# Optimization experiments

Hardware: AMD Instinct MI355X
Metric: run time of the kernel (lower is better)

## Reference

```python
import jax, jax.numpy as jnp
import numpy as np
import math

D_MODEL = 1024
N_HEADS = 16
D_FF = 4096
B, S = 4, 2048
EPS = 1e-5


def _layernorm(x, g, b):
    mu = jnp.mean(x, axis=-1, keepdims=True)
    var = jnp.mean(jnp.square(x - mu), axis=-1, keepdims=True)
    return (x - mu) * jax.lax.rsqrt(var + EPS) * g + b


def setup_inputs() -> dict:
    key = jax.random.key(0)
    ks = jax.random.split(key, 16)
    D, F = D_MODEL, D_FF
    s = 1.0 / math.sqrt(D)
    sf = 1.0 / math.sqrt(F)
    return {
        "x": jax.random.normal(ks[0], (B, S, D), jnp.float32),
        "mask": jnp.ones((B, 1, 1, S), jnp.int32),
        "Wq": jax.random.uniform(ks[1], (D, D), jnp.float32, -s, s),
        "bq": jnp.zeros((D,), jnp.float32),
        "Wk": jax.random.uniform(ks[2], (D, D), jnp.float32, -s, s),
        "bk": jnp.zeros((D,), jnp.float32),
        "Wv": jax.random.uniform(ks[3], (D, D), jnp.float32, -s, s),
        "bv": jnp.zeros((D,), jnp.float32),
        "Wo": jax.random.uniform(ks[4], (D, D), jnp.float32, -s, s),
        "bo": jnp.zeros((D,), jnp.float32),
        "W1": jax.random.uniform(ks[5], (D, F), jnp.float32, -s, s),
        "b1": jnp.zeros((F,), jnp.float32),
        "W2": jax.random.uniform(ks[6], (F, D), jnp.float32, -sf, sf),
        "b2": jnp.zeros((D,), jnp.float32),
        "g1": jnp.ones((D,), jnp.float32),
        "be1": jnp.zeros((D,), jnp.float32),
        "g2": jnp.ones((D,), jnp.float32),
        "be2": jnp.zeros((D,), jnp.float32),
    }


def reference(x, mask, Wq, bq, Wk, bk, Wv, bv, Wo, bo, W1, b1, W2, b2, g1, be1, g2, be2):
    Bb, Ss, D = x.shape
    H = N_HEADS
    hd = D // H
    # QKV projections -> [B, H, S, hd]
    q = (x @ Wq + bq).reshape(Bb, Ss, H, hd).transpose(0, 2, 1, 3)
    k = (x @ Wk + bk).reshape(Bb, Ss, H, hd).transpose(0, 2, 1, 3)
    v = (x @ Wv + bv).reshape(Bb, Ss, H, hd).transpose(0, 2, 1, 3)
    # explicit O(S^2) attention, as in the source
    scores = jnp.einsum("bhqd,bhkd->bhqk", q, k) / math.sqrt(hd)
    scores = jnp.where(mask == 0, jnp.float32(-1e9), scores)
    attn = jax.nn.softmax(scores, axis=-1)
    o = jnp.einsum("bhqk,bhkd->bhqd", attn, v)
    o = o.transpose(0, 2, 1, 3).reshape(Bb, Ss, D)
    attn_out = o @ Wo + bo
    # residual + LN (dropout in eval mode = identity)
    h = _layernorm(x + attn_out, g1, be1)
    ff = jax.nn.relu(h @ W1 + b1) @ W2 + b2
    return _layernorm(h + ff, g2, be2)
```

## Files before the change

kernel.cpp:

```cpp
#include <hip/hip_runtime.h>
#include <hip/hip_bf16.h>
#include <stdint.h>

typedef __bf16 bf16;
typedef __bf16 bf16x8 __attribute__((ext_vector_type(8)));
typedef __bf16 bf16x4 __attribute__((ext_vector_type(4)));
typedef float f32x4 __attribute__((ext_vector_type(4)));
typedef unsigned short u16;

__device__ __forceinline__ float b2f(bf16 v) { return (float)v; }
__device__ __forceinline__ bf16 f2b(float f) { return (bf16)f; }

#define GLD16(gp, lp)                                              \
  __builtin_amdgcn_global_load_lds(                                \
      (const __attribute__((address_space(1))) void*)(gp),         \
      (__attribute__((address_space(3))) void*)(lp), 16, 0, 0)

__device__ __forceinline__ float ldval(const void* p, size_t i, int isf32) {
  return isf32 ? ((const float*)p)[i] : b2f(((const bf16*)p)[i]);
}

__global__ void sniff_kernel(const void* x, int* flag) {
  __shared__ int smax[256];
  int tid = threadIdx.x;
  const u16* p = (const u16*)x;
  int mx = 0;
  for (int i = tid; i < 8192; i += 256) {
    int e = (p[i] >> 7) & 0xFF;
    mx = mx > e ? mx : e;
  }
  smax[tid] = mx;
  __syncthreads();
  for (int s = 128; s > 0; s >>= 1) {
    if (tid < s) smax[tid] = smax[tid] > smax[tid + s] ? smax[tid] : smax[tid + s];
    __syncthreads();
  }
  if (tid == 0) *flag = (smax[0] >= 135) ? 1 : 0;
}

__global__ void cvt_kernel(const void* __restrict__ in, bf16* __restrict__ out,
                           int n, const int* __restrict__ flag) {
  int f = *flag;
  int i = blockIdx.x * 256 + threadIdx.x;
  if (i < n) out[i] = f2b(ldval(in, i, f));
}

__global__ void cvt_biases_kernel(const void* bq, const void* bk, const void* bv,
                                  const void* bo, const void* b1, const void* b2,
                                  const void* g1, const void* be1, const void* g2,
                                  const void* be2, bf16* __restrict__ sv,
                                  const int* __restrict__ flag) {
  int f = *flag;
  int i = blockIdx.x * 256 + threadIdx.x;
  if (i >= 13312) return;
  int seg = i >> 10;
  int off = i & 1023;
  const void* src;
  switch (seg) {
    case 0: src = bq; break;
    case 1: src = bk; break;
    case 2: src = bv; break;
    case 3: src = bo; break;
    case 4: case 5: case 6: case 7: src = b1; off = i - 4096; break;
    case 8: src = b2; break;
    case 9: src = g1; break;
    case 10: src = be1; break;
    case 11: src = g2; break;
    default: src = be2; break;
  }
  sv[i] = f2b(ldval(src, off, f));
}

__global__ void transpose_all(const void* Wq, const void* Wk, const void* Wv,
                              const void* Wo, const void* W1, const void* W2,
                              bf16* WqkvT, bf16* WoT, bf16* W1T, bf16* W2T,
                              const int* __restrict__ flag) {
  int f = *flag;
  __shared__ bf16 tile[32][33];
  int blk = blockIdx.x;
  const void* in; bf16* out; int K, N, bx, by;
  if (blk < 4096) {
    int w = blk >> 10, t = blk & 1023;
    bx = t & 31; by = t >> 5; K = 1024; N = 1024;
    if (w == 0)      { in = Wq; out = WqkvT; }
    else if (w == 1) { in = Wk; out = WqkvT + 1024 * 1024; }
    else if (w == 2) { in = Wv; out = WqkvT + 2048 * 1024; }
    else             { in = Wo; out = WoT; }
  } else if (blk < 8192) {
    int t = blk - 4096; bx = t & 127; by = t >> 7; K = 1024; N = 4096;
    in = W1; out = W1T;
  } else {
    int t = blk - 8192; bx = t & 31; by = t >> 5; K = 4096; N = 1024;
    in = W2; out = W2T;
  }
  int bn = bx * 32, bk = by * 32;
  int tx = threadIdx.x, ty = threadIdx.y;
#pragma unroll
  for (int i = 0; i < 32; i += 8)
    tile[ty + i][tx] = f2b(ldval(in, (size_t)(bk + ty + i) * N + bn + tx, f));
  __syncthreads();
#pragma unroll
  for (int i = 0; i < 32; i += 8)
    out[(size_t)(bn + ty + i) * K + bk + tx] = tile[tx][ty + i];
}

template <int ACT, int GROUP>
__global__ __launch_bounds__(256, 3)
void gemm_bt(const bf16* __restrict__ A, const bf16* __restrict__ Bt,
             const bf16* __restrict__ bias, bf16* __restrict__ C,
             int M, int N, int K) {
  __shared__ __attribute__((aligned(16))) bf16 As[128][64];
  __shared__ __attribute__((aligned(16))) bf16 Bs[128][64];
  __shared__ __attribute__((aligned(16))) bf16 Cs[32][136];
  const int tid = threadIdx.x;
  const int wave = tid >> 6;
  const int lane = tid & 63;

  const int grid_n = N >> 7;
  const int pid = blockIdx.x;
  const int xcd = pid & 7;
  const int j = pid >> 3;
  const int per = GROUP * grid_n;
  const int chunk = j / per;
  const int r0 = j - chunk * per;
  const int mb = xcd * 8 + chunk * GROUP + (r0 & (GROUP - 1));
  const int nb = r0 / GROUP;
  const int m0 = mb * 128;
  const int n0 = nb * 128;

  const int wr = (wave >> 1) * 64;
  const int wc = (wave & 1) * 64;
  const int row_q = lane & 15;
  const int quad = lane >> 4;

  const f32x4 fz = {0.f, 0.f, 0.f, 0.f};
  f32x4 acc[4][4];
#pragma unroll
  for (int i = 0; i < 4; i++)
#pragma unroll
    for (int jj = 0; jj < 4; jj++) acc[i][jj] = fz;

  int srow[4], sck[4];
#pragma unroll
  for (int i = 0; i < 4; i++) {
    int c = i * 256 + tid;
    srow[i] = c >> 3;
    sck[i] = (c & 7) * 8;
  }

  for (int k0 = 0; k0 < K; k0 += 64) {
    __syncthreads();
#pragma unroll
    for (int i = 0; i < 4; i++) {
      GLD16(A + (size_t)(m0 + srow[i]) * K + k0 + sck[i], &As[srow[i]][sck[i]]);
      GLD16(Bt + (size_t)(n0 + srow[i]) * K + k0 + sck[i], &Bs[srow[i]][sck[i]]);
    }
    __syncthreads();
#pragma unroll
    for (int ks = 0; ks < 2; ks++) {
      bf16x8 af[4], bfr[4];
      int cf = ks * 4 + quad;
#pragma unroll
      for (int mi = 0; mi < 4; mi++)
        af[mi] = *(const bf16x8*)&As[wr + mi * 16 + row_q][cf * 8];
#pragma unroll
      for (int ni = 0; ni < 4; ni++)
        bfr[ni] = *(const bf16x8*)&Bs[wc + ni * 16 + row_q][cf * 8];
#pragma unroll
      for (int mi = 0; mi < 4; mi++)
#pragma unroll
        for (int ni = 0; ni < 4; ni++)
          acc[mi][ni] = __builtin_amdgcn_mfma_f32_16x16x32_bf16(
              af[mi], bfr[ni], acc[mi][ni], 0, 0, 0);
    }
  }

#pragma unroll
  for (int p = 0; p < 4; p++) {
    __syncthreads();
    if ((wave >> 1) == (p >> 1)) {
#pragma unroll
      for (int ni = 0; ni < 4; ni++) {
        int col = wc + ni * 16 + row_q;
        float bval = b2f(bias[n0 + col]);
#pragma unroll
        for (int mi2 = 0; mi2 < 2; mi2++) {
          int mi = (p & 1) * 2 + mi2;
#pragma unroll
          for (int reg = 0; reg < 4; reg++) {
            int lr = mi2 * 16 + quad * 4 + reg;
            float v = acc[mi][ni][reg] + bval;
            if (ACT == 1) v = v > 0.f ? v : 0.f;
            Cs[lr][col] = f2b(v);
          }
        }
      }
    }
    __syncthreads();
#pragma unroll
    for (int i = 0; i < 2; i++) {
      int u = i * 256 + tid;
      int row = u >> 4;
      int cu = u & 15;
      uint4 v = *(const uint4*)&Cs[row][cu * 8];
      *(uint4*)&C[(size_t)(m0 + p * 32 + row) * N + n0 + cu * 8] = v;
    }
  }
}

template <int GROUP>
__global__ __launch_bounds__(256, 3)
void gemm_btv(const bf16* __restrict__ A, const bf16* __restrict__ Bt,
              const bf16* __restrict__ bias, bf16* __restrict__ Vg,
              int M, int N, int K) {
  __shared__ __attribute__((aligned(16))) bf16 As[128][64];
  __shared__ __attribute__((aligned(16))) bf16 Bs[128][64];
  __shared__ __attribute__((aligned(16))) bf16 Ct[32][136];
  const int tid = threadIdx.x;
  const int wave = tid >> 6;
  const int lane = tid & 63;

  const int grid_n = N >> 7;
  const int pid = blockIdx.x;
  const int xcd = pid & 7;
  const int j = pid >> 3;
  const int per = GROUP * grid_n;
  const int chunk = j / per;
  const int r0 = j - chunk * per;
  const int mb = xcd * 8 + chunk * GROUP + (r0 & (GROUP - 1));
  const int nb = r0 / GROUP;
  const int m0 = mb * 128;
  const int n0 = nb * 128;

  const int wr = (wave >> 1) * 64;
  const int wc = (wave & 1) * 64;
  const int row_q = lane & 15;
  const int quad = lane >> 4;

  const f32x4 fz = {0.f, 0.f, 0.f, 0.f};
  f32x4 acc[4][4];
#pragma unroll
  for (int i = 0; i < 4; i++)
#pragma unroll
    for (int jj = 0; jj < 4; jj++) acc[i][jj] = fz;

  int srow[4], sck[4];
#pragma unroll
  for (int i = 0; i < 4; i++) {
    int c = i * 256 + tid;
    srow[i] = c >> 3;
    sck[i] = (c & 7) * 8;
  }

  for (int k0 = 0; k0 < K; k0 += 64) {
    __syncthreads();
#pragma unroll
    for (int i = 0; i < 4; i++) {
      GLD16(A + (size_t)(m0 + srow[i]) * K + k0 + sck[i], &As[srow[i]][sck[i]]);
      GLD16(Bt + (size_t)(n0 + srow[i]) * K + k0 + sck[i], &Bs[srow[i]][sck[i]]);
    }
    __syncthreads();
#pragma unroll
    for (int ks = 0; ks < 2; ks++) {
      bf16x8 af[4], bfr[4];
      int cf = ks * 4 + quad;
#pragma unroll
      for (int mi = 0; mi < 4; mi++)
        af[mi] = *(const bf16x8*)&As[wr + mi * 16 + row_q][cf * 8];
#pragma unroll
      for (int ni = 0; ni < 4; ni++)
        bfr[ni] = *(const bf16x8*)&Bs[wc + ni * 16 + row_q][cf * 8];
#pragma unroll
      for (int mi = 0; mi < 4; mi++)
#pragma unroll
        for (int ni = 0; ni < 4; ni++)
          acc[mi][ni] = __builtin_amdgcn_mfma_f32_16x16x32_bf16(
              af[mi], bfr[ni], acc[mi][ni], 0, 0, 0);
    }
  }

  const int b = m0 >> 11;
  const int s0 = m0 & 2047;
#pragma unroll
  for (int p = 0; p < 4; p++) {
    __syncthreads();
    if ((wave & 1) == (p >> 1)) {
#pragma unroll
      for (int ni2 = 0; ni2 < 2; ni2++) {
        int ni = (p & 1) * 2 + ni2;
        int cl = ni2 * 16 + row_q;
        float bval = b2f(bias[n0 + p * 32 + cl]);
#pragma unroll
        for (int mi = 0; mi < 4; mi++)
#pragma unroll
          for (int reg = 0; reg < 4; reg++) {
            int row = wr + mi * 16 + quad * 4 + reg;
            Ct[cl][row] = f2b(acc[mi][ni][reg] + bval);
          }
      }
    }
    __syncthreads();
#pragma unroll
    for (int i = 0; i < 2; i++) {
      int u = i * 256 + tid;
      int cl = u >> 4;
      int rc = u & 15;
      uint4 v = *(const uint4*)&Ct[cl][rc * 8];
      *(uint4*)&Vg[(size_t)(b * 1024 + n0 + p * 32 + cl) * 2048 + s0 + rc * 8] = v;
    }
  }
}

#define BC 128
__global__ __launch_bounds__(256, 3)
void attn_kernel(const bf16* __restrict__ QKb, const bf16* __restrict__ Vg,
                 const int* __restrict__ mask, bf16* __restrict__ O) {
  __shared__ __attribute__((aligned(16))) bf16 Ks[BC][64];
  __shared__ __attribute__((aligned(16))) bf16 Vt[64][128];
  __shared__ __attribute__((aligned(16))) bf16 Ps[4][16][136];
  const int tid = threadIdx.x;
  const int wave = tid >> 6, lane = tid & 63;
  const int pid = blockIdx.x;
  const int xcd = pid & 7;
  const int jj = pid >> 3;
  const int bh = xcd * 8 + (jj >> 5);
  const int b = bh >> 4, h = bh & 15;
  const int q0 = (jj & 31) * 64;
  const int row_q = lane & 15, quad = lane >> 4;

  bf16x8 qf[2];
  {
    int qrow = q0 + wave * 16 + row_q;
    const bf16* qp = QKb + (size_t)(b * 2048 + qrow) * 2048 + h * 64 + quad * 8;
    qf[0] = *(const bf16x8*)qp;
    qf[1] = *(const bf16x8*)(qp + 32);
#pragma unroll
    for (int ks = 0; ks < 2; ks++)
#pragma unroll
      for (int e = 0; e < 8; e++) qf[ks][e] = f2b(b2f(qf[ks][e]) * 0.125f);
  }
  float m_i = -1e30f, l_i = 0.f;
  const f32x4 fz = {0.f, 0.f, 0.f, 0.f};
  f32x4 o_acc[4];
#pragma unroll
  for (int d = 0; d < 4; d++) o_acc[d] = fz;

  int ki[4], kdc[4], ksc[4], vd[4], vkc[4], vsc[4];
#pragma unroll
  for (int j = 0; j < 4; j++) {
    int c = j * 256 + tid;
    ki[j] = c >> 3;  kdc[j] = c & 7;   ksc[j] = (c & 7) ^ (ki[j] & 7);
    vd[j] = c >> 4;  vkc[j] = c & 15;  vsc[j] = (c & 15) ^ (vd[j] & 7);
  }
  const bf16* Kbase = QKb + (size_t)b * 2048 * 2048 + 1024 + h * 64;
  const bf16* Vbase = Vg + (size_t)(b * 1024 + h * 64) * 2048;
  const int* mrow = mask + b * 2048;
  const int swz = row_q & 7;

  for (int kb = 0; kb < 2048 / BC; kb++) {
    __syncthreads();
#pragma unroll
    for (int j = 0; j < 4; j++)
      GLD16(Kbase + (size_t)(kb * BC + ki[j]) * 2048 + ksc[j] * 8,
            &Ks[ki[j]][kdc[j] * 8]);
#pragma unroll
    for (int j = 0; j < 4; j++)
      GLD16(Vbase + (size_t)vd[j] * 2048 + kb * BC + vsc[j] * 8,
            &Vt[vd[j]][vkc[j] * 8]);
    __syncthreads();
    int2 mm = *(const int2*)&mrow[kb * BC + lane * 2];
    bool allok = (__ballot((mm.x != 0) & (mm.y != 0)) == ~0ull);

    f32x4 sacc[8];
#pragma unroll
    for (int nt = 0; nt < 8; nt++) sacc[nt] = fz;
#pragma unroll
    for (int ks = 0; ks < 2; ks++) {
      int kcf = ((ks * 4 + quad) ^ swz) * 8;
#pragma unroll
      for (int nt = 0; nt < 8; nt++) {
        bf16x8 kf = *(const bf16x8*)&Ks[nt * 16 + row_q][kcf];
        sacc[nt] = __builtin_amdgcn_mfma_f32_16x16x32_bf16(kf, qf[ks], sacc[nt], 0, 0, 0);
      }
    }
    if (!allok) {
#pragma unroll
      for (int nt = 0; nt < 8; nt++) {
        int4 m4 = *(const int4*)&mrow[kb * BC + nt * 16 + quad * 4];
#pragma unroll
        for (int r = 0; r < 4; r++)
          if (((const int*)&m4)[r] == 0) sacc[nt][r] = -1e9f;
      }
    }
    float mq[8];
#pragma unroll
    for (int nt = 0; nt < 8; nt++)
      mq[nt] = fmaxf(fmaxf(sacc[nt][0], sacc[nt][1]),
                     fmaxf(sacc[nt][2], sacc[nt][3]));
    float mx = fmaxf(fmaxf(fmaxf(mq[0], mq[1]), fmaxf(mq[2], mq[3])),
                     fmaxf(fmaxf(mq[4], mq[5]), fmaxf(mq[6], mq[7])));
    mx = fmaxf(mx, __shfl_xor(mx, 16));
    mx = fmaxf(mx, __shfl_xor(mx, 32));
    if (!__all(mx - m_i <= 5.0f)) {
      float mnew = fmaxf(m_i, mx);
      float alpha = __expf(m_i - mnew);
      m_i = mnew;
      l_i *= alpha;
      float al[4];
#pragma unroll
      for (int r = 0; r < 4; r++) al[r] = __shfl(alpha, quad * 4 + r);
#pragma unroll
      for (int d = 0; d < 4; d++)
#pragma unroll
        for (int r = 0; r < 4; r++) o_acc[d][r] *= al[r];
    }
    float rs = 0.f;
#pragma unroll
    for (int nt = 0; nt < 8; nt++) {
      float p0 = __expf(sacc[nt][0] - m_i);
      float p1 = __expf(sacc[nt][1] - m_i);
      float p2 = __expf(sacc[nt][2] - m_i);
      float p3 = __expf(sacc[nt][3] - m_i);
      rs += (p0 + p1) + (p2 + p3);
      bf16x4 pv = {f2b(p0), f2b(p1), f2b(p2), f2b(p3)};
      *(bf16x4*)&Ps[wave][row_q][nt * 16 + quad * 4] = pv;
    }
    rs += __shfl_xor(rs, 16);
    rs += __shfl_xor(rs, 32);
    l_i += rs;
#pragma unroll
    for (int kst = 0; kst < 4; kst++) {
      bf16x8 pf = *(const bf16x8*)&Ps[wave][row_q][kst * 32 + quad * 8];
      int vcf = ((kst * 4 + quad) ^ swz) * 8;
#pragma unroll
      for (int d = 0; d < 4; d++) {
        bf16x8 vf = *(const bf16x8*)&Vt[d * 16 + row_q][vcf];
        o_acc[d] = __builtin_amdgcn_mfma_f32_16x16x32_bf16(pf, vf, o_acc[d], 0, 0, 0);
      }
    }
  }
  float lv[4];
#pragma unroll
  for (int r = 0; r < 4; r++) lv[r] = __shfl(l_i, quad * 4 + r);
#pragma unroll
  for (int d = 0; d < 4; d++) {
#pragma unroll
    for (int r = 0; r < 4; r++) {
      int row = q0 + wave * 16 + quad * 4 + r;
      float v = o_acc[d][r] / fmaxf(lv[r], 1e-20f);
      O[(size_t)(b * 2048 + row) * 1024 + h * 64 + d * 16 + row_q] = f2b(v);
    }
  }
}

__global__ __launch_bounds__(256)
void ln_kernel(const bf16* __restrict__ a, const bf16* __restrict__ res,
               const bf16* __restrict__ g, const bf16* __restrict__ be,
               bf16* __restrict__ out) {
  const int row = blockIdx.x;
  const int tid = threadIdx.x;
  __shared__ float red[8];
  float xs[4], sum = 0.f, sq = 0.f;
  const size_t base = (size_t)row * 1024;
#pragma unroll
  for (int i = 0; i < 4; i++) {
    int idx = i * 256 + tid;
    float x = b2f(a[base + idx]) + b2f(res[base + idx]);
    xs[i] = x; sum += x; sq += x * x;
  }
#pragma unroll
  for (int off = 1; off < 64; off <<= 1) {
    sum += __shfl_xor(sum, off);
    sq += __shfl_xor(sq, off);
  }
  int wave = tid >> 6, lane = tid & 63;
  if (lane == 0) { red[wave] = sum; red[4 + wave] = sq; }
  __syncthreads();
  sum = red[0] + red[1] + red[2] + red[3];
  sq = red[4] + red[5] + red[6] + red[7];
  float mu = sum * (1.f / 1024.f);
  float var = sq * (1.f / 1024.f) - mu * mu;
  float rstd = rsqrtf(fmaxf(var, 0.f) + 1e-5f);
#pragma unroll
  for (int i = 0; i < 4; i++) {
    int idx = i * 256 + tid;
    float y = (xs[i] - mu) * rstd * b2f(g[idx]) + b2f(be[idx]);
    out[base + idx] = f2b(y);
  }
}

__global__ __launch_bounds__(256)
void ln_out_kernel(const bf16* __restrict__ a, const bf16* __restrict__ res,
                   const bf16* __restrict__ g, const bf16* __restrict__ be,
                   void* __restrict__ out, const int* __restrict__ flag) {
  const int f = *flag;
  const int row = blockIdx.x;
  const int tid = threadIdx.x;
  __shared__ float red[8];
  float xs[4], sum = 0.f, sq = 0.f;
  const size_t base = (size_t)row * 1024;
#pragma unroll
  for (int i = 0; i < 4; i++) {
    int idx = i * 256 + tid;
    float x = b2f(a[base + idx]) + b2f(res[base + idx]);
    xs[i] = x; sum += x; sq += x * x;
  }
#pragma unroll
  for (int off = 1; off < 64; off <<= 1) {
    sum += __shfl_xor(sum, off);
    sq += __shfl_xor(sq, off);
  }
  int wave = tid >> 6, lane = tid & 63;
  if (lane == 0) { red[wave] = sum; red[4 + wave] = sq; }
  __syncthreads();
  sum = red[0] + red[1] + red[2] + red[3];
  sq = red[4] + red[5] + red[6] + red[7];
  float mu = sum * (1.f / 1024.f);
  float var = sq * (1.f / 1024.f) - mu * mu;
  float rstd = rsqrtf(fmaxf(var, 0.f) + 1e-5f);
#pragma unroll
  for (int i = 0; i < 4; i++) {
    int idx = i * 256 + tid;
    float y = (xs[i] - mu) * rstd * b2f(g[idx]) + b2f(be[idx]);
    if (f) ((float*)out)[base + idx] = y;
    else   ((bf16*)out)[base + idx] = f2b(y);
  }
}

extern "C" void kernel_launch(void* const* d_in, const int* in_sizes, int n_in,
                              void* d_out, int out_size, void* d_ws, size_t ws_size,
                              hipStream_t stream) {
  (void)in_sizes; (void)n_in; (void)out_size; (void)ws_size;
  const void* x   = d_in[0];
  const int* mask = (const int*)d_in[1];
  const void* Wq  = d_in[2];
  const void* bq  = d_in[3];
  const void* Wk  = d_in[4];
  const void* bk  = d_in[5];
  const void* Wv  = d_in[6];
  const void* bv  = d_in[7];
  const void* Wo  = d_in[8];
  const void* bo  = d_in[9];
  const void* W1  = d_in[10];
  const void* b1  = d_in[11];
  const void* W2  = d_in[12];
  const void* b2  = d_in[13];
  const void* g1  = d_in[14];
  const void* be1 = d_in[15];
  const void* g2  = d_in[16];
  const void* be2 = d_in[17];

  char* ws = (char*)d_ws;
  bf16* xb    = (bf16*)(ws + 0);
  bf16* WqkvT = (bf16*)(ws + 16777216);
  bf16* WoT   = (bf16*)(ws + 23068672);
  bf16* W1T   = (bf16*)(ws + 25165824);
  bf16* W2T   = (bf16*)(ws + 33554432);
  bf16* sv    = (bf16*)(ws + 41943040);
  bf16* bqkvB = sv;
  bf16* boB   = sv + 3072;
  bf16* b1B   = sv + 4096;
  bf16* b2B   = sv + 8192;
  bf16* g1B   = sv + 9216;
  bf16* be1B  = sv + 10240;
  bf16* g2B   = sv + 11264;
  bf16* be2B  = sv + 12288;
  int*  flag  = (int*)(ws + 41943040 + 26624);
  bf16* QKb   = (bf16*)(ws + 41975808);
  bf16* Vg    = (bf16*)(ws + 75530240);
  bf16* Obuf  = (bf16*)(ws + 92307456);
  bf16* hbuf  = (bf16*)(ws + 109084672);
  bf16* attnp = (bf16*)(ws + 41975808);
  bf16* ff1   = (bf16*)(ws + 41975808);
  bf16* ff2o  = (bf16*)(ws + 0);

  sniff_kernel<<<1, 256, 0, stream>>>(x, flag);

  cvt_kernel<<<32768, 256, 0, stream>>>(x, xb, 8388608, flag);
  cvt_biases_kernel<<<52, 256, 0, stream>>>(bq, bk, bv, bo, b1, b2, g1, be1,
                                            g2, be2, sv, flag);

  dim3 tb(32, 8);
  transpose_all<<<12288, tb, 0, stream>>>(Wq, Wk, Wv, Wo, W1, W2,
                                          WqkvT, WoT, W1T, W2T, flag);

  gemm_bt<0, 8><<<1024, 256, 0, stream>>>(xb, WqkvT, bqkvB, QKb, 8192, 2048, 1024);
  gemm_btv<8><<<512, 256, 0, stream>>>(xb, WqkvT + 2048 * 1024, bqkvB + 2048, Vg,
                                       8192, 1024, 1024);
  attn_kernel<<<2048, 256, 0, stream>>>(QKb, Vg, mask, Obuf);
  gemm_bt<0, 8><<<512, 256, 0, stream>>>(Obuf, WoT, boB, attnp, 8192, 1024, 1024);
  ln_kernel<<<8192, 256, 0, stream>>>(xb, attnp, g1B, be1B, hbuf);
  gemm_bt<1, 8><<<2048, 256, 0, stream>>>(hbuf, W1T, b1B, ff1, 8192, 4096, 1024);
  gemm_bt<0, 4><<<512, 256, 0, stream>>>(ff1, W2T, b2B, ff2o, 8192, 1024, 4096);
  ln_out_kernel<<<8192, 256, 0, stream>>>(hbuf, ff2o, g2B, be2B, d_out, flag);
}
```

Baseline: 615.7 us.

## Double-buffer K/V tiles in attention kernel and swizzle P staging

The attention kernel now keeps two LDS buffers for K and V. The next tile's global-to-LDS loads are issued before computing on the current tile, so load latency overlaps with the MFMA and softmax work, and there is one barrier per iteration instead of two. Per-tile mask ballots are computed once up front into a bitmask, and the P staging buffer uses an XOR swizzle in place of padding to avoid bank conflicts. Launch bounds drop from 3 to 2 blocks per CU because of the larger LDS footprint, which lowers occupancy.

```diff
diff --git a/kernel.cpp b/kernel.cpp
--- a/kernel.cpp
+++ b/kernel.cpp
@@ -312,12 +312,13 @@
 }
 
 #define BC 128
-__global__ __launch_bounds__(256, 3)
+#define NKT 16
+__global__ __launch_bounds__(256, 2)
 void attn_kernel(const bf16* __restrict__ QKb, const bf16* __restrict__ Vg,
                  const int* __restrict__ mask, bf16* __restrict__ O) {
-  __shared__ __attribute__((aligned(16))) bf16 Ks[BC][64];
-  __shared__ __attribute__((aligned(16))) bf16 Vt[64][128];
-  __shared__ __attribute__((aligned(16))) bf16 Ps[4][16][136];
+  __shared__ __attribute__((aligned(16))) bf16 Ks[2][BC][64];
+  __shared__ __attribute__((aligned(16))) bf16 Vt[2][64][BC];
+  __shared__ __attribute__((aligned(16))) bf16 Ps[4][16][128];
   const int tid = threadIdx.x;
   const int wave = tid >> 6, lane = tid & 63;
   const int pid = blockIdx.x;
@@ -357,19 +358,34 @@
   const int* mrow = mask + b * 2048;
   const int swz = row_q & 7;
 
-  for (int kb = 0; kb < 2048 / BC; kb++) {
-    __syncthreads();
-#pragma unroll
-    for (int j = 0; j < 4; j++)
-      GLD16(Kbase + (size_t)(kb * BC + ki[j]) * 2048 + ksc[j] * 8,
-            &Ks[ki[j]][kdc[j] * 8]);
-#pragma unroll
-    for (int j = 0; j < 4; j++)
-      GLD16(Vbase + (size_t)vd[j] * 2048 + kb * BC + vsc[j] * 8,
-            &Vt[vd[j]][vkc[j] * 8]);
-    __syncthreads();
+  unsigned int allmask = 0;
+  for (int kb = 0; kb < NKT; kb++) {
     int2 mm = *(const int2*)&mrow[kb * BC + lane * 2];
-    bool allok = (__ballot((mm.x != 0) & (mm.y != 0)) == ~0ull);
+    if (__ballot((mm.x != 0) & (mm.y != 0)) == ~0ull) allmask |= (1u << kb);
+  }
+
+#pragma unroll
+  for (int j = 0; j < 4; j++)
+    GLD16(Kbase + (size_t)ki[j] * 2048 + ksc[j] * 8, &Ks[0][ki[j]][kdc[j] * 8]);
+#pragma unroll
+  for (int j = 0; j < 4; j++)
+    GLD16(Vbase + (size_t)vd[j] * 2048 + vsc[j] * 8, &Vt[0][vd[j]][vkc[j] * 8]);
+
+  for (int kb = 0; kb < NKT; kb++) {
+    const int cur = kb & 1;
+    __syncthreads();
+    if (kb + 1 < NKT) {
+      const int nbuf = cur ^ 1;
+      const size_t koff = (size_t)(kb + 1) * BC;
+#pragma unroll
+      for (int j = 0; j < 4; j++)
+        GLD16(Kbase + (koff + ki[j]) * 2048 + ksc[j] * 8,
+              &Ks[nbuf][ki[j]][kdc[j] * 8]);
+#pragma unroll
+      for (int j = 0; j < 4; j++)
+        GLD16(Vbase + (size_t)vd[j] * 2048 + koff + vsc[j] * 8,
+              &Vt[nbuf][vd[j]][vkc[j] * 8]);
+    }
 
     f32x4 sacc[8];
 #pragma unroll
@@ -379,11 +395,11 @@
       int kcf = ((ks * 4 + quad) ^ swz) * 8;
 #pragma unroll
       for (int nt = 0; nt < 8; nt++) {
-        bf16x8 kf = *(const bf16x8*)&Ks[nt * 16 + row_q][kcf];
+        bf16x8 kf = *(const bf16x8*)&Ks[cur][nt * 16 + row_q][kcf];
         sacc[nt] = __builtin_amdgcn_mfma_f32_16x16x32_bf16(kf, qf[ks], sacc[nt], 0, 0, 0);
       }
     }
-    if (!allok) {
+    if (!((allmask >> kb) & 1u)) {
 #pragma unroll
       for (int nt = 0; nt < 8; nt++) {
         int4 m4 = *(const int4*)&mrow[kb * BC + nt * 16 + quad * 4];
@@ -423,18 +439,19 @@
       float p3 = __expf(sacc[nt][3] - m_i);
       rs += (p0 + p1) + (p2 + p3);
       bf16x4 pv = {f2b(p0), f2b(p1), f2b(p2), f2b(p3)};
-      *(bf16x4*)&Ps[wave][row_q][nt * 16 + quad * 4] = pv;
+      int gsw = (((nt * 2 + (quad >> 1)) ^ swz) << 3) + ((quad & 1) << 2);
+      *(bf16x4*)&Ps[wave][row_q][gsw] = pv;
     }
     rs += __shfl_xor(rs, 16);
     rs += __shfl_xor(rs, 32);
     l_i += rs;
 #pragma unroll
     for (int kst = 0; kst < 4; kst++) {
-      bf16x8 pf = *(const bf16x8*)&Ps[wave][row_q][kst * 32 + quad * 8];
-      int vcf = ((kst * 4 + quad) ^ swz) * 8;
+      int cf = ((kst * 4 + quad) ^ swz) * 8;
+      bf16x8 pf = *(const bf16x8*)&Ps[wave][row_q][cf];
 #pragma unroll
       for (int d = 0; d < 4; d++) {
-        bf16x8 vf = *(const bf16x8*)&Vt[d * 16 + row_q][vcf];
+        bf16x8 vf = *(const bf16x8*)&Vt[cur][d * 16 + row_q][cf];
         o_acc[d] = __builtin_amdgcn_mfma_f32_16x16x32_bf16(pf, vf, o_acc[d], 0, 0, 0);
       }
     }
```

Result: slower. 633.9 us (+3.0%).
